# Performance work log

Measured on AMD Instinct MI355X. Metric: run time of the kernel, lower is better.

## Reference

```python
import jax, jax.numpy as jnp
import numpy as np

N_NODES = 50000
N_EDGES = 800000
X_DIM, H_DIM, Y_DIM = 128, 256, 128


def spmm(adj_vals, adj_row, adj_col, x):
    # sparse [N,N] @ dense [N,D] via gather + segment scatter-add
    msgs = adj_vals[:, None] * x[adj_col]  # [E, D]
    return jax.ops.segment_sum(msgs, adj_row, num_segments=N_NODES)


def setup_inputs() -> dict:
    key = jax.random.key(0)
    ks = jax.random.split(key, 6)
    x = jax.random.uniform(ks[0], (N_NODES, X_DIM), dtype=jnp.float32)
    adj_vals = jax.random.uniform(ks[1], (N_EDGES,), dtype=jnp.float32)
    adj_row = jax.random.randint(ks[2], (N_EDGES,), 0, N_NODES, dtype=jnp.int32)
    adj_col = jax.random.randint(ks[3], (N_EDGES,), 0, N_NODES, dtype=jnp.int32)
    W1 = jax.random.normal(ks[4], (X_DIM, H_DIM), dtype=jnp.float32) * (1.0 / np.sqrt(X_DIM))
    b1 = jnp.zeros((H_DIM,), dtype=jnp.float32)
    W2 = jax.random.normal(ks[5], (H_DIM, Y_DIM), dtype=jnp.float32) * (1.0 / np.sqrt(H_DIM))
    b2 = jnp.zeros((Y_DIM,), dtype=jnp.float32)
    return {"x": x, "adj_vals": adj_vals, "adj_row": adj_row, "adj_col": adj_col,
            "W1": W1, "b1": b1, "W2": W2, "b2": b2}


def reference(x, adj_vals, adj_row, adj_col, W1, b1, W2, b2):
    # row-normalize features: x / (sum_j x_ij + 1e-4)
    x = x / (jnp.sum(x, axis=1, keepdims=True) + 1e-4)
    # layer 1: spmm -> linear -> relu (dropout is identity at eval)
    h = jax.nn.relu(spmm(adj_vals, adj_row, adj_col, x) @ W1 + b1)  # [N, H]
    # layer 2: spmm -> linear
    y = spmm(adj_vals, adj_row, adj_col, h) @ W2 + b2  # [N, Y]
    return y
```

## Files before the change

### kernel.cpp

```cpp
#include <hip/hip_runtime.h>

#define N_NODES 50000
#define N_EDGES 800000
#define X_DIM 128
#define H_DIM 256
#define Y_DIM 128

typedef unsigned int uint32;
typedef unsigned short ushort16;
typedef __attribute__((ext_vector_type(8))) short short8;
typedef __attribute__((ext_vector_type(4))) float floatx4;

__device__ inline ushort16 f2bf(float f) {
    uint32 u = __float_as_uint(f);
    return (ushort16)((u + 0x7FFFu + ((u >> 16) & 1u)) >> 16);
}
__device__ inline float bf_lo(uint32 u) { return __uint_as_float(u << 16); }
__device__ inline float bf_hi(uint32 u) { return __uint_as_float(u & 0xFFFF0000u); }

#define NORM_BLOCKS 12500
#define CONV_BLOCKS 256
#define ZERO_BLOCKS 196

#define BUCKET_SHIFT 7
#define NB 391
#define PASSA_CHUNK 8192
#define PASSA_BLOCKS 98
#define CAP_B 2560

__global__ __launch_bounds__(256) void prep_kernel(
    const float* __restrict__ x, uint32* __restrict__ xb,
    const float* __restrict__ W1, const float* __restrict__ W2,
    ushort16* __restrict__ W1t, ushort16* __restrict__ W2t,
    int* __restrict__ counts) {
    int b = blockIdx.x;
    if (b < NORM_BLOCKS) {
        int row = (b * 256 + threadIdx.x) >> 6;
        int lane = threadIdx.x & 63;
        float2 v = ((const float2*)x)[(size_t)row * 64 + lane];
        float s = v.x + v.y;
        #pragma unroll
        for (int off = 32; off > 0; off >>= 1) s += __shfl_xor(s, off, 64);
        float inv = 1.0f / (s + 1e-4f);
        uint32 lo = (uint32)f2bf(v.x * inv);
        uint32 hi = (uint32)f2bf(v.y * inv);
        xb[(size_t)row * 64 + lane] = lo | (hi << 16);
    } else if (b < NORM_BLOCKS + CONV_BLOCKS) {
        int t = (b - NORM_BLOCKS) * 256 + threadIdx.x;
        if (t < X_DIM * H_DIM) {
            int n = t >> 7, k = t & 127;
            W1t[t] = f2bf(W1[k * H_DIM + n]);
        } else {
            int u = t - X_DIM * H_DIM;
            int y = u >> 8, k = u & 255;
            W2t[u] = f2bf(W2[k * Y_DIM + y]);
        }
    } else {
        int i = (b - NORM_BLOCKS - CONV_BLOCKS) * 256 + threadIdx.x;
        if (i < N_NODES) counts[i] = 0;
    }
}

__global__ __launch_bounds__(256) void hist_kernel(
    const int* __restrict__ rows, int* __restrict__ counts) {
    int e = blockIdx.x * blockDim.x + threadIdx.x;
    if (e < N_EDGES) atomicAdd(&counts[rows[e]], 1);
}

#define SCAN_BLOCKS 196

__global__ __launch_bounds__(256) void scan_partial_kernel(
    const int* __restrict__ counts, int* __restrict__ partials) {
    __shared__ int wsum[4];
    int t = threadIdx.x;
    int i = blockIdx.x * 256 + t;
    int s = (i < N_NODES) ? counts[i] : 0;
    #pragma unroll
    for (int off = 32; off > 0; off >>= 1) s += __shfl_down(s, off, 64);
    if ((t & 63) == 0) wsum[t >> 6] = s;
    __syncthreads();
    if (t == 0) partials[blockIdx.x] = wsum[0] + wsum[1] + wsum[2] + wsum[3];
}

__global__ __launch_bounds__(256) void scan_apply_kernel(
    const int* __restrict__ counts, const int* __restrict__ partials,
    int* __restrict__ rowptr, int* __restrict__ bucket_cursor) {
    __shared__ int red[256];
    __shared__ int part[256];
    int t = threadIdx.x;
    int i = blockIdx.x * 256 + t;
    red[t] = (t < blockIdx.x) ? partials[t] : 0;
    int v = (i < N_NODES) ? counts[i] : 0;
    part[t] = v;
    __syncthreads();
    #pragma unroll
    for (int off = 128; off > 0; off >>= 1) {
        if (t < off) red[t] += red[t + off];
        __syncthreads();
    }
    int block_off = red[0];
    #pragma unroll
    for (int off = 1; off < 256; off <<= 1) {
        int u = (t >= off) ? part[t - off] : 0;
        __syncthreads();
        part[t] += u;
        __syncthreads();
    }
    if (i < N_NODES) {
        int rp = block_off + part[t] - v;
        rowptr[i] = rp;
        if ((i & 127) == 0) bucket_cursor[i >> BUCKET_SHIFT] = rp;
    }
    if (blockIdx.x == 0 && t == 0) rowptr[N_NODES] = N_EDGES;
}

__global__ __launch_bounds__(512) void bucketize_kernel(
    const int* __restrict__ rows, const int* __restrict__ cols,
    const float* __restrict__ vals, int* __restrict__ bucket_cursor,
    int2* __restrict__ edges) {
    __shared__ int h[512];
    __shared__ int o[512];
    __shared__ int c[NB];
    __shared__ int g[NB];
    __shared__ int2 buf[PASSA_CHUNK];
    int t = threadIdx.x;
    int base = blockIdx.x * PASSA_CHUNK;
    int M = N_EDGES - base; if (M > PASSA_CHUNK) M = PASSA_CHUNK;
    h[t] = 0;
    __syncthreads();
    #pragma unroll
    for (int k = 0; k < PASSA_CHUNK / 512; k++) {
        int e = base + t + k * 512;
        if (e < N_EDGES) atomicAdd(&h[rows[e] >> BUCKET_SHIFT], 1);
    }
    __syncthreads();
    int val = h[t];
    #pragma unroll
    for (int off = 1; off < 512; off <<= 1) {
        int u = (t >= off) ? h[t - off] : 0;
        __syncthreads();
        h[t] += u;
        __syncthreads();
    }
    o[t] = h[t] - val;
    if (t < NB) {
        c[t] = 0;
        g[t] = (val > 0) ? atomicAdd(&bucket_cursor[t], val) : 0;
    }
    __syncthreads();
    #pragma unroll
    for (int k = 0; k < PASSA_CHUNK / 512; k++) {
        int e = base + t + k * 512;
        if (e < N_EDGES) {
            int r = rows[e];
            int b = r >> BUCKET_SHIFT;
            int p = o[b] + atomicAdd(&c[b], 1);
            buf[p] = make_int2(cols[e] | ((r & 127) << 16) | (b << 23),
                               __float_as_int(vals[e]));
        }
    }
    __syncthreads();
    for (int i = t; i < M; i += 512) {
        int2 e = buf[i];
        int b = (int)((uint32)e.x >> 23);
        edges[g[b] + (i - o[b])] = e;
    }
}

__global__ __launch_bounds__(256) void bucket_sort_kernel(
    const int* __restrict__ rowptr, int2* __restrict__ edges,
    int2* __restrict__ scratch) {
    __shared__ int2 buf[CAP_B];
    __shared__ int2 buf2[CAP_B];
    __shared__ int h[128], o[128], c[128];
    int b = blockIdx.x, t = threadIdx.x;
    int base = rowptr[b << BUCKET_SHIFT];
    int hi = (b + 1) << BUCKET_SHIFT; if (hi > N_NODES) hi = N_NODES;
    int cnt = rowptr[hi] - base;
    bool fits = (cnt <= CAP_B);
    if (t < 128) h[t] = 0;
    __syncthreads();
    for (int i = t; i < cnt; i += 256) {
        int2 e = edges[base + i];
        if (fits) buf[i] = e; else scratch[base + i] = e;
        atomicAdd(&h[(e.x >> 16) & 127], 1);
    }
    __syncthreads();
    int valh = (t < 128) ? h[t] : 0;
    #pragma unroll
    for (int off = 1; off < 128; off <<= 1) {
        int u = (t >= off && t < 128) ? h[t - off] : 0;
        __syncthreads();
        if (t < 128) h[t] += u;
        __syncthreads();
    }
    if (t < 128) { o[t] = h[t] - valh; c[t] = 0; }
    __syncthreads();
    for (int i = t; i < cnt; i += 256) {
        int2 e = fits ? buf[i] : scratch[base + i];
        int lr = (e.x >> 16) & 127;
        int p = o[lr] + atomicAdd(&c[lr], 1);
        if (fits) buf2[p] = e; else edges[base + p] = e;
    }
    __syncthreads();
    if (fits)
        for (int i = t; i < cnt; i += 256) edges[base + i] = buf2[i];
}

template <bool OUT_F32>
__global__ __launch_bounds__(256) void spmm_csr_bf16(
    const uint32* __restrict__ feat, const int* __restrict__ rowptr,
    const int2* __restrict__ edges, const float* __restrict__ bias,
    void* __restrict__ outv) {
    int row = (blockIdx.x * blockDim.x + threadIdx.x) >> 6;
    int lane = threadIdx.x & 63;
    if (row >= N_NODES) return;
    int start = rowptr[row], end = rowptr[row + 1];
    float ax0 = 0.f, ay0 = 0.f, ax1 = 0.f, ay1 = 0.f;
    float ax2 = 0.f, ay2 = 0.f, ax3 = 0.f, ay3 = 0.f;
    for (int base = start; base < end; base += 64) {
        int n = end - base; if (n > 64) n = 64;
        int2 ev = make_int2(0, 0);
        if (lane < n) ev = edges[base + lane];
        int c = ev.x & 0xFFFF; float v = __int_as_float(ev.y);
        int j = 0;
        for (; j + 8 <= n; j += 8) {
            int c0 = __shfl(c, j, 64), c1 = __shfl(c, j + 1, 64);
            int c2 = __shfl(c, j + 2, 64), c3 = __shfl(c, j + 3, 64);
            int c4 = __shfl(c, j + 4, 64), c5 = __shfl(c, j + 5, 64);
            int c6 = __shfl(c, j + 6, 64), c7 = __shfl(c, j + 7, 64);
            float v0 = __shfl(v, j, 64), v1 = __shfl(v, j + 1, 64);
            float v2 = __shfl(v, j + 2, 64), v3 = __shfl(v, j + 3, 64);
            float v4 = __shfl(v, j + 4, 64), v5 = __shfl(v, j + 5, 64);
            float v6 = __shfl(v, j + 6, 64), v7 = __shfl(v, j + 7, 64);
            uint32 f0 = feat[(size_t)c0 * 64 + lane];
            uint32 f1 = feat[(size_t)c1 * 64 + lane];
            uint32 f2 = feat[(size_t)c2 * 64 + lane];
            uint32 f3 = feat[(size_t)c3 * 64 + lane];
            uint32 f4 = feat[(size_t)c4 * 64 + lane];
            uint32 f5 = feat[(size_t)c5 * 64 + lane];
            uint32 f6 = feat[(size_t)c6 * 64 + lane];
            uint32 f7 = feat[(size_t)c7 * 64 + lane];
            ax0 += v0 * bf_lo(f0); ay0 += v0 * bf_hi(f0);
            ax1 += v1 * bf_lo(f1); ay1 += v1 * bf_hi(f1);
            ax2 += v2 * bf_lo(f2); ay2 += v2 * bf_hi(f2);
            ax3 += v3 * bf_lo(f3); ay3 += v3 * bf_hi(f3);
            ax0 += v4 * bf_lo(f4); ay0 += v4 * bf_hi(f4);
            ax1 += v5 * bf_lo(f5); ay1 += v5 * bf_hi(f5);
            ax2 += v6 * bf_lo(f6); ay2 += v6 * bf_hi(f6);
            ax3 += v7 * bf_lo(f7); ay3 += v7 * bf_hi(f7);
        }
        for (; j + 4 <= n; j += 4) {
            int c0 = __shfl(c, j, 64), c1 = __shfl(c, j + 1, 64);
            int c2 = __shfl(c, j + 2, 64), c3 = __shfl(c, j + 3, 64);
            float v0 = __shfl(v, j, 64), v1 = __shfl(v, j + 1, 64);
            float v2 = __shfl(v, j + 2, 64), v3 = __shfl(v, j + 3, 64);
            uint32 f0 = feat[(size_t)c0 * 64 + lane];
            uint32 f1 = feat[(size_t)c1 * 64 + lane];
            uint32 f2 = feat[(size_t)c2 * 64 + lane];
            uint32 f3 = feat[(size_t)c3 * 64 + lane];
            ax0 += v0 * bf_lo(f0); ay0 += v0 * bf_hi(f0);
            ax1 += v1 * bf_lo(f1); ay1 += v1 * bf_hi(f1);
            ax2 += v2 * bf_lo(f2); ay2 += v2 * bf_hi(f2);
            ax3 += v3 * bf_lo(f3); ay3 += v3 * bf_hi(f3);
        }
        for (; j < n; j++) {
            int c0 = __shfl(c, j, 64);
            float v0 = __shfl(v, j, 64);
            uint32 f0 = feat[(size_t)c0 * 64 + lane];
            ax0 += v0 * bf_lo(f0); ay0 += v0 * bf_hi(f0);
        }
    }
    float ax = (ax0 + ax1) + (ax2 + ax3);
    float ay = (ay0 + ay1) + (ay2 + ay3);
    if (OUT_F32) {
        float2 b = ((const float2*)bias)[lane];
        ((float2*)outv)[(size_t)row * 64 + lane] = make_float2(ax + b.x, ay + b.y);
    } else {
        ((uint32*)outv)[(size_t)row * 64 + lane] =
            (uint32)f2bf(ax) | ((uint32)f2bf(ay) << 16);
    }
}

__global__ __launch_bounds__(256, 3) void gemm_fused(
    const uint32* __restrict__ agg1, const ushort16* __restrict__ W1t,
    const ushort16* __restrict__ W2t, const float* __restrict__ b1,
    ushort16* __restrict__ hw, int nrows) {
    __shared__ ushort16 a_s[64 * 136];
    __shared__ ushort16 h_s[64 * 264];
    const int tx = threadIdx.x;
    const int wave = tx >> 6, lane = tx & 63;
    const int quad = lane >> 4, l16 = lane & 15;
    const int row0 = blockIdx.x * 64;

    short8 bfr1[4][4];
    #pragma unroll
    for (int ct = 0; ct < 4; ct++)
        #pragma unroll
        for (int kk = 0; kk < 4; kk++)
            bfr1[ct][kk] = *(const short8*)
                &W1t[(wave * 64 + ct * 16 + l16) * 128 + kk * 32 + quad * 8];

    #pragma unroll
    for (int i = 0; i < 16; i++) {
        int idx = tx + i * 256;
        int r = idx >> 6, c = idx & 63;
        uint32 v = 0;
        if (row0 + r < nrows) v = agg1[(size_t)(row0 + r) * 64 + c];
        *(uint32*)&a_s[r * 136 + c * 2] = v;
    }
    __syncthreads();

    floatx4 acc1[4][4];
    #pragma unroll
    for (int rs = 0; rs < 4; rs++)
        #pragma unroll
        for (int ct = 0; ct < 4; ct++)
            #pragma unroll
            for (int j = 0; j < 4; j++) acc1[rs][ct][j] = 0.f;
    #pragma unroll
    for (int kk = 0; kk < 4; kk++) {
        #pragma unroll
        for (int rs = 0; rs < 4; rs++) {
            short8 af = *(const short8*)&a_s[(rs * 16 + l16) * 136 + kk * 32 + quad * 8];
            #pragma unroll
            for (int ct = 0; ct < 4; ct++)
                acc1[rs][ct] = __builtin_amdgcn_mfma_f32_16x16x32_bf16(
                    af, bfr1[ct][kk], acc1[rs][ct], 0, 0, 0);
        }
    }
    float bv[4];
    #pragma unroll
    for (int ct = 0; ct < 4; ct++) bv[ct] = b1[wave * 64 + ct * 16 + l16];
    #pragma unroll
    for (int rs = 0; rs < 4; rs++)
        #pragma unroll
        for (int ct = 0; ct < 4; ct++)
            #pragma unroll
            for (int reg = 0; reg < 4; reg++) {
                float v = acc1[rs][ct][reg] + bv[ct];
                v = v > 0.f ? v : 0.f;
                h_s[(rs * 16 + quad * 4 + reg) * 264 + wave * 64 + ct * 16 + l16] = f2bf(v);
            }

    short8 bfr2[2][8];
    #pragma unroll
    for (int ct = 0; ct < 2; ct++)
        #pragma unroll
        for (int kk = 0; kk < 8; kk++)
            bfr2[ct][kk] = *(const short8*)
                &W2t[(wave * 32 + ct * 16 + l16) * 256 + kk * 32 + quad * 8];
    __syncthreads();

    floatx4 acc2[4][2];
    #pragma unroll
    for (int rs = 0; rs < 4; rs++)
        #pragma unroll
        for (int ct = 0; ct < 2; ct++)
            #pragma unroll
            for (int j = 0; j < 4; j++) acc2[rs][ct][j] = 0.f;
    #pragma unroll
    for (int kk = 0; kk < 8; kk++) {
        #pragma unroll
        for (int rs = 0; rs < 4; rs++) {
            short8 af = *(const short8*)&h_s[(rs * 16 + l16) * 264 + kk * 32 + quad * 8];
            #pragma unroll
            for (int ct = 0; ct < 2; ct++)
                acc2[rs][ct] = __builtin_amdgcn_mfma_f32_16x16x32_bf16(
                    af, bfr2[ct][kk], acc2[rs][ct], 0, 0, 0);
        }
    }
    #pragma unroll
    for (int rs = 0; rs < 4; rs++)
        #pragma unroll
        for (int ct = 0; ct < 2; ct++)
            #pragma unroll
            for (int reg = 0; reg < 4; reg++) {
                int row = row0 + rs * 16 + quad * 4 + reg;
                if (row < nrows)
                    hw[(size_t)row * 128 + wave * 32 + ct * 16 + l16] =
                        f2bf(acc2[rs][ct][reg]);
            }
}

extern "C" void kernel_launch(void* const* d_in, const int* in_sizes, int n_in,
                              void* d_out, int out_size, void* d_ws, size_t ws_size,
                              hipStream_t stream) {
    const float* x = (const float*)d_in[0];
    const float* adj_vals = (const float*)d_in[1];
    const int* adj_row = (const int*)d_in[2];
    const int* adj_col = (const int*)d_in[3];
    const float* W1 = (const float*)d_in[4];
    const float* b1 = (const float*)d_in[5];
    const float* W2 = (const float*)d_in[6];
    const float* b2 = (const float*)d_in[7];
    float* out = (float*)d_out;

    char* ws = (char*)d_ws;
    uint32*   xb       = (uint32*)  (ws + 0);
    uint32*   agg1     = (uint32*)  (ws + 12800000);
    ushort16* hw       = (ushort16*)(ws + 25600000);
    int2*     edges    = (int2*)    (ws + 38400000);
    int2*     scratch  = (int2*)    (ws + 44800000);
    int*      counts   = (int*)     (ws + 51200000);
    int*      rowptr   = (int*)     (ws + 51400192);
    int*      partials = (int*)     (ws + 51600896);
    int*      bcursor  = (int*)     (ws + 51601792);
    ushort16* W1t      = (ushort16*)(ws + 51603456);
    ushort16* W2t      = (ushort16*)(ws + 51668992);

    hipLaunchKernelGGL(prep_kernel, dim3(NORM_BLOCKS + CONV_BLOCKS + ZERO_BLOCKS),
                       dim3(256), 0, stream, x, xb, W1, W2, W1t, W2t, counts);

    hipLaunchKernelGGL(hist_kernel, dim3((N_EDGES + 255) / 256), dim3(256),
                       0, stream, adj_row, counts);
    hipLaunchKernelGGL(scan_partial_kernel, dim3(SCAN_BLOCKS), dim3(256),
                       0, stream, counts, partials);
    hipLaunchKernelGGL(scan_apply_kernel, dim3(SCAN_BLOCKS), dim3(256),
                       0, stream, counts, partials, rowptr, bcursor);

    hipLaunchKernelGGL(bucketize_kernel, dim3(PASSA_BLOCKS), dim3(512),
                       0, stream, adj_row, adj_col, adj_vals, bcursor, edges);
    hipLaunchKernelGGL(bucket_sort_kernel, dim3(NB), dim3(256),
                       0, stream, rowptr, edges, scratch);

    hipLaunchKernelGGL((spmm_csr_bf16<false>), dim3((N_NODES * 64 + 255) / 256), dim3(256),
                       0, stream, xb, rowptr, edges, (const float*)nullptr, (void*)agg1);

    hipLaunchKernelGGL(gemm_fused, dim3((N_NODES + 63) / 64), dim3(256),
                       0, stream, agg1, W1t, W2t, b1, hw, N_NODES);

    hipLaunchKernelGGL((spmm_csr_bf16<true>), dim3((N_NODES * 64 + 255) / 256), dim3(256),
                       0, stream, (const uint32*)hw, rowptr, edges, b2, (void*)out);
}
```

Before: 253.0 us.

## Replace per-node histogram and scans with per-chunk bucket histograms

Removes the global per-node atomic histogram and the two-kernel node scan. Per-chunk bucket histograms are now computed inside the prep kernel, a single-block kernel scans the bucket totals, and rowptr is derived inside the bucket sort from its local per-row histogram. This cuts two kernel launches and 800K global atomics, and halves the bucketize chunk size to double the block count. In exchange there is a serial single-block scan over a 196x391 partial table.

```diff
diff --git a/kernel.cpp b/kernel.cpp
--- a/kernel.cpp
+++ b/kernel.cpp
@@ -18,21 +18,20 @@
 __device__ inline float bf_lo(uint32 u) { return __uint_as_float(u << 16); }
 __device__ inline float bf_hi(uint32 u) { return __uint_as_float(u & 0xFFFF0000u); }
 
+#define BUCKET_SHIFT 7
+#define NB 391
+#define CHUNK 4096
+#define NCHUNK 196
+#define CAP_B 2560
+
 #define NORM_BLOCKS 12500
 #define CONV_BLOCKS 256
-#define ZERO_BLOCKS 196
-
-#define BUCKET_SHIFT 7
-#define NB 391
-#define PASSA_CHUNK 8192
-#define PASSA_BLOCKS 98
-#define CAP_B 2560
 
 __global__ __launch_bounds__(256) void prep_kernel(
     const float* __restrict__ x, uint32* __restrict__ xb,
     const float* __restrict__ W1, const float* __restrict__ W2,
     ushort16* __restrict__ W1t, ushort16* __restrict__ W2t,
-    int* __restrict__ counts) {
+    const int* __restrict__ rows, int* __restrict__ gpartial) {
     int b = blockIdx.x;
     if (b < NORM_BLOCKS) {
         int row = (b * 256 + threadIdx.x) >> 6;
@@ -56,127 +55,105 @@
             W2t[u] = f2bf(W2[k * Y_DIM + y]);
         }
     } else {
-        int i = (b - NORM_BLOCKS - CONV_BLOCKS) * 256 + threadIdx.x;
-        if (i < N_NODES) counts[i] = 0;
-    }
-}
-
-__global__ __launch_bounds__(256) void hist_kernel(
-    const int* __restrict__ rows, int* __restrict__ counts) {
-    int e = blockIdx.x * blockDim.x + threadIdx.x;
-    if (e < N_EDGES) atomicAdd(&counts[rows[e]], 1);
-}
-
-#define SCAN_BLOCKS 196
-
-__global__ __launch_bounds__(256) void scan_partial_kernel(
-    const int* __restrict__ counts, int* __restrict__ partials) {
-    __shared__ int wsum[4];
+        __shared__ int h[NB];
+        int j = b - NORM_BLOCKS - CONV_BLOCKS;
+        int t = threadIdx.x;
+        for (int i = t; i < NB; i += 256) h[i] = 0;
+        __syncthreads();
+        int base = j * CHUNK;
+        #pragma unroll
+        for (int k = 0; k < CHUNK / 256; k++) {
+            int e = base + t + k * 256;
+            if (e < N_EDGES) atomicAdd(&h[rows[e] >> BUCKET_SHIFT], 1);
+        }
+        __syncthreads();
+        for (int i = t; i < NB; i += 256) gpartial[j * NB + i] = h[i];
+    }
+}
+
+__global__ __launch_bounds__(512) void bucket_scan_kernel(
+    const int* __restrict__ gpartial, int* __restrict__ bucket_base,
+    int* __restrict__ bcursor, int* __restrict__ rowptr) {
+    __shared__ int s[512];
     int t = threadIdx.x;
-    int i = blockIdx.x * 256 + t;
-    int s = (i < N_NODES) ? counts[i] : 0;
-    #pragma unroll
-    for (int off = 32; off > 0; off >>= 1) s += __shfl_down(s, off, 64);
-    if ((t & 63) == 0) wsum[t >> 6] = s;
-    __syncthreads();
-    if (t == 0) partials[blockIdx.x] = wsum[0] + wsum[1] + wsum[2] + wsum[3];
-}
-
-__global__ __launch_bounds__(256) void scan_apply_kernel(
-    const int* __restrict__ counts, const int* __restrict__ partials,
-    int* __restrict__ rowptr, int* __restrict__ bucket_cursor) {
-    __shared__ int red[256];
-    __shared__ int part[256];
-    int t = threadIdx.x;
-    int i = blockIdx.x * 256 + t;
-    red[t] = (t < blockIdx.x) ? partials[t] : 0;
-    int v = (i < N_NODES) ? counts[i] : 0;
-    part[t] = v;
-    __syncthreads();
-    #pragma unroll
-    for (int off = 128; off > 0; off >>= 1) {
-        if (t < off) red[t] += red[t + off];
-        __syncthreads();
-    }
-    int block_off = red[0];
-    #pragma unroll
-    for (int off = 1; off < 256; off <<= 1) {
-        int u = (t >= off) ? part[t - off] : 0;
-        __syncthreads();
-        part[t] += u;
-        __syncthreads();
-    }
-    if (i < N_NODES) {
-        int rp = block_off + part[t] - v;
-        rowptr[i] = rp;
-        if ((i & 127) == 0) bucket_cursor[i >> BUCKET_SHIFT] = rp;
-    }
-    if (blockIdx.x == 0 && t == 0) rowptr[N_NODES] = N_EDGES;
+    int total = 0;
+    if (t < NB) {
+        #pragma unroll 4
+        for (int j = 0; j < NCHUNK; j++) total += gpartial[j * NB + t];
+    }
+    s[t] = total;
+    __syncthreads();
+    #pragma unroll
+    for (int off = 1; off < 512; off <<= 1) {
+        int u = (t >= off) ? s[t - off] : 0;
+        __syncthreads();
+        s[t] += u;
+        __syncthreads();
+    }
+    if (t < NB) {
+        int excl = s[t] - total;
+        bucket_base[t] = excl;
+        bcursor[t] = excl;
+    }
+    if (t == 0) { bucket_base[NB] = N_EDGES; rowptr[N_NODES] = N_EDGES; }
 }
 
 __global__ __launch_bounds__(512) void bucketize_kernel(
     const int* __restrict__ rows, const int* __restrict__ cols,
-    const float* __restrict__ vals, int* __restrict__ bucket_cursor,
-    int2* __restrict__ edges) {
-    __shared__ int h[512];
-    __shared__ int o[512];
+    const float* __restrict__ vals, const int* __restrict__ gpartial,
+    int* __restrict__ bcursor, int2* __restrict__ edges) {
+    __shared__ int ob[512];
     __shared__ int c[NB];
     __shared__ int g[NB];
-    __shared__ int2 buf[PASSA_CHUNK];
+    __shared__ int2 buf[CHUNK];
     int t = threadIdx.x;
-    int base = blockIdx.x * PASSA_CHUNK;
-    int M = N_EDGES - base; if (M > PASSA_CHUNK) M = PASSA_CHUNK;
-    h[t] = 0;
-    __syncthreads();
-    #pragma unroll
-    for (int k = 0; k < PASSA_CHUNK / 512; k++) {
-        int e = base + t + k * 512;
-        if (e < N_EDGES) atomicAdd(&h[rows[e] >> BUCKET_SHIFT], 1);
-    }
-    __syncthreads();
-    int val = h[t];
+    int j = blockIdx.x;
+    int base = j * CHUNK;
+    int M = N_EDGES - base; if (M > CHUNK) M = CHUNK;
+    int cnt = (t < NB) ? gpartial[j * NB + t] : 0;
+    ob[t] = cnt;
+    __syncthreads();
     #pragma unroll
     for (int off = 1; off < 512; off <<= 1) {
-        int u = (t >= off) ? h[t - off] : 0;
-        __syncthreads();
-        h[t] += u;
-        __syncthreads();
-    }
-    o[t] = h[t] - val;
+        int u = (t >= off) ? ob[t - off] : 0;
+        __syncthreads();
+        ob[t] += u;
+        __syncthreads();
+    }
+    ob[t] -= cnt;
     if (t < NB) {
         c[t] = 0;
-        g[t] = (val > 0) ? atomicAdd(&bucket_cursor[t], val) : 0;
-    }
-    __syncthreads();
-    #pragma unroll
-    for (int k = 0; k < PASSA_CHUNK / 512; k++) {
+        g[t] = (cnt > 0) ? atomicAdd(&bcursor[t], cnt) : 0;
+    }
+    __syncthreads();
+    #pragma unroll
+    for (int k = 0; k < CHUNK / 512; k++) {
         int e = base + t + k * 512;
         if (e < N_EDGES) {
             int r = rows[e];
-            int b = r >> BUCKET_SHIFT;
-            int p = o[b] + atomicAdd(&c[b], 1);
-            buf[p] = make_int2(cols[e] | ((r & 127) << 16) | (b << 23),
+            int bb = r >> BUCKET_SHIFT;
+            int p = ob[bb] + atomicAdd(&c[bb], 1);
+            buf[p] = make_int2(cols[e] | ((r & 127) << 16) | (bb << 23),
                                __float_as_int(vals[e]));
         }
     }
     __syncthreads();
     for (int i = t; i < M; i += 512) {
         int2 e = buf[i];
-        int b = (int)((uint32)e.x >> 23);
-        edges[g[b] + (i - o[b])] = e;
+        int bb = (int)((uint32)e.x >> 23);
+        edges[g[bb] + (i - ob[bb])] = e;
     }
 }
 
 __global__ __launch_bounds__(256) void bucket_sort_kernel(
-    const int* __restrict__ rowptr, int2* __restrict__ edges,
-    int2* __restrict__ scratch) {
+    const int* __restrict__ bucket_base, int2* __restrict__ edges,
+    int2* __restrict__ scratch, int* __restrict__ rowptr) {
     __shared__ int2 buf[CAP_B];
     __shared__ int2 buf2[CAP_B];
     __shared__ int h[128], o[128], c[128];
     int b = blockIdx.x, t = threadIdx.x;
-    int base = rowptr[b << BUCKET_SHIFT];
-    int hi = (b + 1) << BUCKET_SHIFT; if (hi > N_NODES) hi = N_NODES;
-    int cnt = rowptr[hi] - base;
+    int base = bucket_base[b];
+    int cnt = bucket_base[b + 1] - base;
     bool fits = (cnt <= CAP_B);
     if (t < 128) h[t] = 0;
     __syncthreads();
@@ -194,7 +171,12 @@
         if (t < 128) h[t] += u;
         __syncthreads();
     }
-    if (t < 128) { o[t] = h[t] - valh; c[t] = 0; }
+    if (t < 128) {
+        o[t] = h[t] - valh;
+        c[t] = 0;
+        int i = (b << BUCKET_SHIFT) + t;
+        if (i < N_NODES) rowptr[i] = base + h[t] - valh;
+    }
     __syncthreads();
     for (int i = t; i < cnt; i += 256) {
         int2 e = fits ? buf[i] : scratch[base + i];
@@ -402,27 +384,24 @@
     ushort16* hw       = (ushort16*)(ws + 25600000);
     int2*     edges    = (int2*)    (ws + 38400000);
     int2*     scratch  = (int2*)    (ws + 44800000);
-    int*      counts   = (int*)     (ws + 51200000);
-    int*      rowptr   = (int*)     (ws + 51400192);
-    int*      partials = (int*)     (ws + 51600896);
-    int*      bcursor  = (int*)     (ws + 51601792);
-    ushort16* W1t      = (ushort16*)(ws + 51603456);
-    ushort16* W2t      = (ushort16*)(ws + 51668992);
-
-    hipLaunchKernelGGL(prep_kernel, dim3(NORM_BLOCKS + CONV_BLOCKS + ZERO_BLOCKS),
-                       dim3(256), 0, stream, x, xb, W1, W2, W1t, W2t, counts);
-
-    hipLaunchKernelGGL(hist_kernel, dim3((N_EDGES + 255) / 256), dim3(256),
-                       0, stream, adj_row, counts);
-    hipLaunchKernelGGL(scan_partial_kernel, dim3(SCAN_BLOCKS), dim3(256),
-                       0, stream, counts, partials);
-    hipLaunchKernelGGL(scan_apply_kernel, dim3(SCAN_BLOCKS), dim3(256),
-                       0, stream, counts, partials, rowptr, bcursor);
-
-    hipLaunchKernelGGL(bucketize_kernel, dim3(PASSA_BLOCKS), dim3(512),
-                       0, stream, adj_row, adj_col, adj_vals, bcursor, edges);
+    int*      gpartial = (int*)     (ws + 51200000);
+    int*      rowptr   = (int*)     (ws + 51513344);
+    int*      bbase    = (int*)     (ws + 51714048);
+    int*      bcursor  = (int*)     (ws + 51716096);
+    ushort16* W1t      = (ushort16*)(ws + 51718144);
+    ushort16* W2t      = (ushort16*)(ws + 51783680);
+
+    hipLaunchKernelGGL(prep_kernel, dim3(NORM_BLOCKS + CONV_BLOCKS + NCHUNK),
+                       dim3(256), 0, stream, x, xb, W1, W2, W1t, W2t,
+                       adj_row, gpartial);
+
+    hipLaunchKernelGGL(bucket_scan_kernel, dim3(1), dim3(512),
+                       0, stream, gpartial, bbase, bcursor, rowptr);
+
+    hipLaunchKernelGGL(bucketize_kernel, dim3(NCHUNK), dim3(512),
+                       0, stream, adj_row, adj_col, adj_vals, gpartial, bcursor, edges);
     hipLaunchKernelGGL(bucket_sort_kernel, dim3(NB), dim3(256),
-                       0, stream, rowptr, edges, scratch);
+                       0, stream, bbase, edges, scratch, rowptr);
 
     hipLaunchKernelGGL((spmm_csr_bf16<false>), dim3((N_NODES * 64 + 255) / 256), dim3(256),
                        0, stream, xb, rowptr, edges, (const float*)nullptr, (void*)agg1);
```

Result: faster. 223.8 us (-11.5%).
